# Kernel optimization log

Measured on AMD Instinct MI355X. Metric: run time of the kernel, lower is better.

The kernel has to match this reference:

```python
import jax, jax.numpy as jnp
from jax import lax
import numpy as np

CONF = 0.05   # score threshold
IOU = 0.5     # NMS IoU threshold
IMG = 512.0   # input image size (d0)
PRE_K = 1000  # fixed pre-NMS candidate count (replaces variable-length boolean mask)
MAX_DET = 100 # fixed max detections per image
B, C = 16, 90
CLS_OFF = 4096.0  # batched_nms class offset (> max coordinate)

def _make_anchors():
    # EfficientDet-d0 anchor grid: strides 8..128, anchor_scale=4, 3 scales x 3 ratios
    strides = [8, 16, 32, 64, 128]
    scs = [2.0 ** 0, 2.0 ** (1.0 / 3.0), 2.0 ** (2.0 / 3.0)]
    ratios = [(1.0, 1.0), (1.4, 0.7), (0.7, 1.4)]
    out = []
    for s in strides:
        n = int(512 // s)
        yy, xx = np.meshgrid((np.arange(n) + 0.5) * s, (np.arange(n) + 0.5) * s, indexing='ij')
        cy = yy.reshape(-1); cx = xx.reshape(-1)
        for sc in scs:
            for ry, rx in ratios:
                h = 4.0 * s * sc * ry / 2.0
                w = 4.0 * s * sc * rx / 2.0
                out.append(np.stack([cy - h, cx - w, cy + h, cx + w], -1))  # (y1,x1,y2,x2)
    return jnp.asarray(np.concatenate(out, 0), dtype=jnp.float32)[None]  # [1,49104,4]

def setup_inputs():
    key = jax.random.key(0)
    k1, k2 = jax.random.split(key)
    anchors = _make_anchors()
    A = anchors.shape[1]
    regression = 0.1 * jax.random.normal(k1, (B, A, 4), dtype=jnp.float32)
    classification = jax.random.uniform(k2, (B, A, C), dtype=jnp.float32) ** 8  # sigmoid-like sparse scores
    scales = jnp.ones((B, 2), dtype=jnp.float32)
    pads = jnp.zeros((B, 2), dtype=jnp.float32)
    return {'anchors': anchors, 'regression': regression, 'classification': classification,
            'scales': scales, 'pads': pads}

def _decode(anchors, regression):
    yca = (anchors[..., 0] + anchors[..., 2]) / 2
    xca = (anchors[..., 1] + anchors[..., 3]) / 2
    ha = anchors[..., 2] - anchors[..., 0]
    wa = anchors[..., 3] - anchors[..., 1]
    w = jnp.exp(regression[..., 3]) * wa
    h = jnp.exp(regression[..., 2]) * ha
    yc = regression[..., 0] * ha + yca
    xc = regression[..., 1] * wa + xca
    return jnp.stack([xc - w / 2, yc - h / 2, xc + w / 2, yc + h / 2], axis=2)  # [B,A,4] xyxy

def _iou_mat(b):
    # b: [K,4] xyxy -> [K,K] IoU
    area = jnp.clip(b[:, 2] - b[:, 0], 0) * jnp.clip(b[:, 3] - b[:, 1], 0)
    lt = jnp.maximum(b[:, None, :2], b[None, :, :2])
    rb = jnp.minimum(b[:, None, 2:], b[None, :, 2:])
    wh = jnp.clip(rb - lt, 0)
    inter = wh[..., 0] * wh[..., 1]
    return inter / jnp.maximum(area[:, None] + area[None, :] - inter, 1e-8)

def _nms_keep(boxes, scores):
    # greedy NMS on score-sorted boxes; entries with score<=CONF never kept nor suppress
    K = boxes.shape[0]
    iou = _iou_mat(boxes)
    valid = scores > CONF
    idx = jnp.arange(K)
    def body(i, keep):
        cur = keep[i] & valid[i]
        sup = cur & (iou[i] > IOU) & (idx > i)
        return keep & ~sup
    return lax.fori_loop(0, K, body, valid)

def _per_image(boxes, smax, cls, scale, pad):
    # boxes [A,4], smax [A], cls [A], scale [2] (sy,sx), pad [2] (py,px)
    sc = jnp.where(smax > CONF, smax, -1.0)
    topv, topi = lax.top_k(sc, PRE_K)          # sorted descending
    bk = boxes[topi]                            # [K,4]
    ck = cls[topi]                              # [K]
    boff = bk + (ck.astype(bk.dtype) * CLS_OFF)[:, None]  # class-aware NMS offset
    keep = lax.stop_gradient(_nms_keep(lax.stop_gradient(boff), lax.stop_gradient(topv)))
    sf = jnp.where(keep, topv, -1.0)
    fv, fi = lax.top_k(sf, MAX_DET)
    bf = bk[fi]
    lf = ck[fi]
    valid = fv > CONF
    # undo pad/scale, clip to image (original clips to orig width/height; identity scale/pad here)
    x1 = jnp.clip((bf[:, 0] - pad[1]) / scale[1], 0.0, IMG)
    y1 = jnp.clip((bf[:, 1] - pad[0]) / scale[0], 0.0, IMG)
    x2 = jnp.clip((bf[:, 2] - pad[1]) / scale[1], 0.0, IMG)
    y2 = jnp.clip((bf[:, 3] - pad[0]) / scale[0], 0.0, IMG)
    bfr = jnp.stack([x1, y1, x2, y2], -1)
    bfr = jnp.where(valid[:, None], bfr, 0.0)
    sv = jnp.where(valid, fv, 0.0)
    lfv = jnp.where(valid, lf, -1)
    return bfr, sv, lfv

def reference(anchors, regression, classification, scales, pads):
    boxes = _decode(anchors, regression)            # [B,A,4]
    smax = jnp.max(classification, axis=2)          # [B,A]
    cls = jnp.argmax(classification, axis=2)        # [B,A]
    bf, sv, lf = jax.vmap(_per_image)(boxes, smax, cls, scales, pads)
    out5 = jnp.concatenate([bf, sv[..., None]], axis=-1)  # [B,MAX_DET,5]
    return out5, lf
```

## Files before the change

kernel.cpp:

```cpp
#include <hip/hip_runtime.h>

#define A_N 49104
#define B_N 16
#define C_N 90
#define KP 1024
#define MROWS 1088

__global__ __launch_bounds__(256) void k_score(
    const float* __restrict__ classification,
    float* __restrict__ smax, int* __restrict__ cls) {
  int a = blockIdx.x * 256 + threadIdx.x;
  int b = blockIdx.y;
  if (a >= A_N) return;
  const float2* cp2 = (const float2*)(classification + ((size_t)b * A_N + a) * C_N);
  float m = -1.0f; int am = 0;
#pragma unroll
  for (int k = 0; k < C_N / 2; ++k) {
    float2 v = cp2[k];
    if (v.x > m) { m = v.x; am = 2 * k; }
    if (v.y > m) { m = v.y; am = 2 * k + 1; }
  }
  size_t o = (size_t)b * A_N + a;
  smax[o] = m;
  cls[o] = am;
}

__global__ __launch_bounds__(1024) void k_select(
    const float* __restrict__ smax, const int* __restrict__ cls,
    const float* __restrict__ anchors, const float* __restrict__ regression,
    float* __restrict__ topbox, float* __restrict__ topv, int* __restrict__ topcls,
    unsigned long long* __restrict__ validb) {
  __shared__ unsigned long long cand[2048];
  __shared__ unsigned s_red[16];
  __shared__ unsigned s_tot;
  __shared__ int s_cnt;
  const int tid = threadIdx.x;
  const int b = blockIdx.x;
  const int lane = tid & 63, wv = tid >> 6;
  const float* sm = smax + (size_t)b * A_N;

  unsigned ub[48];
#pragma unroll
  for (int k = 0; k < 48; ++k) {
    int a = tid + k * 1024;
    float s = (a < A_N) ? sm[a] : -1.0f;
    ub[k] = (s > 0.05f) ? __float_as_uint(s) : 0u;
  }

  unsigned lo = __float_as_uint(0.05f) + 1u;
  unsigned hi = __float_as_uint(1.0f) + 1u;
  while (hi - lo > 1u) {
    unsigned mid = lo + ((hi - lo) >> 1);
    int c = 0;
#pragma unroll
    for (int k = 0; k < 48; ++k) c += (ub[k] >= mid) ? 1 : 0;
#pragma unroll
    for (int off = 32; off > 0; off >>= 1) c += __shfl_down(c, off, 64);
    if (lane == 0) s_red[wv] = (unsigned)c;
    __syncthreads();
    if (tid == 0) {
      unsigned tot = 0;
      for (int i = 0; i < 16; ++i) tot += s_red[i];
      s_tot = tot;
    }
    __syncthreads();
    if (s_tot >= 1000u) lo = mid; else hi = mid;
    __syncthreads();
  }
  const unsigned T = lo;

  if (tid == 0) s_cnt = 0;
  __syncthreads();
#pragma unroll
  for (int k = 0; k < 48; ++k) {
    if (ub[k] >= T) {
      int a = tid + k * 1024;
      int p = atomicAdd(&s_cnt, 1);
      if (p < 2048)
        cand[p] = ~(((unsigned long long)ub[k] << 32) |
                    (unsigned long long)(0xFFFFFFFFu - (unsigned)a));
    }
  }
  __syncthreads();
  int cnt = s_cnt; if (cnt > 2048) cnt = 2048;
  for (int i = tid; i < 2048; i += 1024) if (i >= cnt) cand[i] = ~0ULL;
  __syncthreads();

  for (int k = 2; k <= 2048; k <<= 1) {
    for (int j = k >> 1; j > 0; j >>= 1) {
      for (int i = tid; i < 2048; i += 1024) {
        int l = i ^ j;
        if (l > i) {
          unsigned long long vi = cand[i], vl = cand[l];
          if ((vi > vl) == ((i & k) == 0)) { cand[i] = vl; cand[l] = vi; }
        }
      }
      __syncthreads();
    }
  }

  {
    const int t = tid;
    unsigned long long key = ~cand[t];
    unsigned sb = (unsigned)(key >> 32);
    unsigned idxa = 0xFFFFFFFFu - (unsigned)(key & 0xFFFFFFFFull);
    bool v = (t < 1000) && (sb != 0u);
    float b0 = 0.f, b1 = 0.f, b2 = 0.f, b3 = 0.f, sv = -1.0f; int cl = 0;
    if (v) {
      float4 an = ((const float4*)anchors)[idxa];
      float4 rg = ((const float4*)regression)[(size_t)b * A_N + idxa];
      float yca = __fmul_rn(__fadd_rn(an.x, an.z), 0.5f);
      float xca = __fmul_rn(__fadd_rn(an.y, an.w), 0.5f);
      float ha = __fsub_rn(an.z, an.x);
      float wa = __fsub_rn(an.w, an.y);
      float w  = __fmul_rn((float)exp((double)rg.w), wa);
      float h  = __fmul_rn((float)exp((double)rg.z), ha);
      float yc = __fadd_rn(__fmul_rn(rg.x, ha), yca);
      float xc = __fadd_rn(__fmul_rn(rg.y, wa), xca);
      float wh = __fmul_rn(w, 0.5f), hh = __fmul_rn(h, 0.5f);
      b0 = __fsub_rn(xc, wh); b1 = __fsub_rn(yc, hh);
      b2 = __fadd_rn(xc, wh); b3 = __fadd_rn(yc, hh);
      cl = cls[(size_t)b * A_N + idxa];
      sv = __uint_as_float(sb);
    }
    float* tb = topbox + ((size_t)b * KP + t) * 4;
    tb[0] = b0; tb[1] = b1; tb[2] = b2; tb[3] = b3;
    topv[b * KP + t] = sv;
    topcls[b * KP + t] = cl;
  }
  if (tid < 16) {
    unsigned long long vb = 0ULL;
    for (int bit = 0; bit < 64; ++bit) {
      int t = tid * 64 + bit;
      if (t < 1000 && (unsigned)((~cand[t]) >> 32) != 0u) vb |= (1ULL << bit);
    }
    validb[b * 16 + tid] = vb;
  }
}

__global__ __launch_bounds__(256) void k_mask(
    const float* __restrict__ topbox, const int* __restrict__ topcls,
    unsigned long long* __restrict__ mask) {
  __shared__ float sx1[KP], sy1[KP], sx2[KP], sy2[KP], sar[KP];
  const int b = blockIdx.y, rb = blockIdx.x;
  const int tid = threadIdx.x;
  for (int jj = tid; jj < KP; jj += 256) {
    const float* bp = topbox + ((size_t)b * KP + jj) * 4;
    float off = (float)topcls[b * KP + jj] * 4096.0f;
    float x1 = __fadd_rn(bp[0], off), y1 = __fadd_rn(bp[1], off);
    float x2 = __fadd_rn(bp[2], off), y2 = __fadd_rn(bp[3], off);
    sx1[jj] = x1; sy1[jj] = y1; sx2[jj] = x2; sy2[jj] = y2;
    sar[jj] = __fmul_rn(fmaxf(__fsub_rn(x2, x1), 0.0f), fmaxf(__fsub_rn(y2, y1), 0.0f));
  }
  __syncthreads();
  const int wv = tid >> 6, lane = tid & 63;
  for (int task = wv; task < 128; task += 4) {
    const int r = task >> 4, cc = task & 15;
    const int i = rb * 8 + r;
    const int j = cc * 64 + lane;
    float xi1 = sx1[i], yi1 = sy1[i], xi2 = sx2[i], yi2 = sy2[i], ai = sar[i];
    float ltx = fmaxf(xi1, sx1[j]);
    float lty = fmaxf(yi1, sy1[j]);
    float rbx = fminf(xi2, sx2[j]);
    float rby = fminf(yi2, sy2[j]);
    float wx = fmaxf(__fsub_rn(rbx, ltx), 0.0f);
    float wy = fmaxf(__fsub_rn(rby, lty), 0.0f);
    float inter = __fmul_rn(wx, wy);
    float uni = fmaxf(__fsub_rn(__fadd_rn(ai, sar[j]), inter), 1e-8f);
    bool pred = (__fdiv_rn(inter, uni) > 0.5f) && (j > i) && (j < 1000);
    unsigned long long m = __ballot(pred);
    if (lane == 0) mask[((size_t)b * MROWS + i) * 16 + cc] = m;
  }
}

__global__ __launch_bounds__(64) void k_greedy(
    const unsigned long long* __restrict__ mask,
    const float* __restrict__ topv, const float* __restrict__ topbox,
    const int* __restrict__ topcls, const unsigned long long* __restrict__ validb,
    const float* __restrict__ scales, const float* __restrict__ pads,
    float* __restrict__ out) {
  const int b = blockIdx.x;
  const int lane = threadIdx.x;
  const int c = lane & 15, q = lane >> 4;
  const unsigned long long* M = mask + (size_t)b * MROWS * 16;
  unsigned long long remv = ~validb[b * 16 + c];
  unsigned long long ring[16];
#pragma unroll
  for (int t = 0; t < 16; ++t) ring[t] = M[(size_t)(t * 4 + q) * 16 + c];
  __shared__ unsigned long long keepw[16];
  __shared__ int sel[100];
  __shared__ int s_cnt;
#pragma unroll 1
  for (int g = 0; g < 16; ++g) {
#pragma unroll
    for (int t = 0; t < 16; ++t) {
      const int bb = g * 16 + t;
      unsigned long long cur = ring[t];
      ring[t] = M[(size_t)((bb + 16) * 4 + q) * 16 + c];
#pragma unroll
      for (int q2 = 0; q2 < 4; ++q2) {
        const int i = bb * 4 + q2;
        unsigned long long w = __shfl(remv, i >> 6, 64);
        bool kept = ((w >> (i & 63)) & 1ULL) == 0ULL;
        unsigned long long srow = __shfl(cur, q2 * 16 + c, 64);
        if (kept) remv |= srow;
      }
    }
  }
  if (q == 0) keepw[c] = (~remv) & validb[b * 16 + c];
  __syncthreads();
  if (lane == 0) {
    int cnt = 0;
    for (int ci = 0; ci < 16 && cnt < 100; ++ci) {
      unsigned long long w = keepw[ci];
      while (w && cnt < 100) {
        int bit = __builtin_ctzll(w);
        sel[cnt++] = ci * 64 + bit;
        w &= (w - 1ULL);
      }
    }
    s_cnt = cnt;
  }
  __syncthreads();
  const float sy = scales[b * 2 + 0], sxx = scales[b * 2 + 1];
  const float py = pads[b * 2 + 0],  px = pads[b * 2 + 1];
  for (int s = lane; s < 100; s += 64) {
    float o0 = 0, o1 = 0, o2 = 0, o3 = 0, o4 = 0, lf = -1.0f;
    if (s < s_cnt) {
      const int i = sel[s];
      const float* bp = topbox + ((size_t)b * KP + i) * 4;
      o0 = fminf(fmaxf(__fdiv_rn(__fsub_rn(bp[0], px), sxx), 0.0f), 512.0f);
      o1 = fminf(fmaxf(__fdiv_rn(__fsub_rn(bp[1], py), sy ), 0.0f), 512.0f);
      o2 = fminf(fmaxf(__fdiv_rn(__fsub_rn(bp[2], px), sxx), 0.0f), 512.0f);
      o3 = fminf(fmaxf(__fdiv_rn(__fsub_rn(bp[3], py), sy ), 0.0f), 512.0f);
      o4 = topv[b * KP + i];
      lf = (float)topcls[b * KP + i];
    }
    float* op = out + ((size_t)b * 100 + s) * 5;
    op[0] = o0; op[1] = o1; op[2] = o2; op[3] = o3; op[4] = o4;
    out[(size_t)B_N * 500 + b * 100 + s] = lf;
  }
}

extern "C" void kernel_launch(void* const* d_in, const int* in_sizes, int n_in,
                              void* d_out, int out_size, void* d_ws, size_t ws_size,
                              hipStream_t stream) {
  const float* anchors        = (const float*)d_in[0];
  const float* regression     = (const float*)d_in[1];
  const float* classification = (const float*)d_in[2];
  const float* scales         = (const float*)d_in[3];
  const float* pads           = (const float*)d_in[4];
  char* ws = (char*)d_ws;
  float* smax   = (float*)(ws + 0);
  int*   cls    = (int*)  (ws + 3142656);
  float* topbox = (float*)(ws + 6285312);
  float* topv   = (float*)(ws + 6547456);
  int*   topcls = (int*)  (ws + 6612992);
  unsigned long long* validb = (unsigned long long*)(ws + 6678528);
  unsigned long long* mask   = (unsigned long long*)(ws + 6680576);
  float* out = (float*)d_out;

  k_score <<<dim3((A_N + 255) / 256, B_N), 256, 0, stream>>>(classification, smax, cls);
  k_select<<<B_N, 1024, 0, stream>>>(smax, cls, anchors, regression, topbox, topv, topcls, validb);
  k_mask  <<<dim3(125, B_N), 256, 0, stream>>>(topbox, topcls, mask);
  k_greedy<<<B_N, 64, 0, stream>>>(mask, topv, topbox, topcls, validb, scales, pads, out);
}
```

Before: 540.4 us.

## Coalesce score loads via shared tiles and replace threshold bisection with radix histogram

```diff
diff --git a/kernel.cpp b/kernel.cpp
--- a/kernel.cpp
+++ b/kernel.cpp
@@ -5,24 +5,36 @@
 #define C_N 90
 #define KP 1024
 #define MROWS 1088
+#define ANCH 128
 
 __global__ __launch_bounds__(256) void k_score(
     const float* __restrict__ classification,
     float* __restrict__ smax, int* __restrict__ cls) {
-  int a = blockIdx.x * 256 + threadIdx.x;
-  int b = blockIdx.y;
-  if (a >= A_N) return;
-  const float2* cp2 = (const float2*)(classification + ((size_t)b * A_N + a) * C_N);
-  float m = -1.0f; int am = 0;
-#pragma unroll
-  for (int k = 0; k < C_N / 2; ++k) {
-    float2 v = cp2[k];
-    if (v.x > m) { m = v.x; am = 2 * k; }
-    if (v.y > m) { m = v.y; am = 2 * k + 1; }
-  }
-  size_t o = (size_t)b * A_N + a;
-  smax[o] = m;
-  cls[o] = am;
+  __shared__ float sc[ANCH * C_N];
+  const int blk = blockIdx.x, b = blockIdx.y;
+  const int base = blk * ANCH;
+  const int nA = min(ANCH, A_N - base);
+  const int nf4 = (nA * C_N) >> 2;
+  const float4* s4 = (const float4*)(classification + ((size_t)b * A_N + base) * C_N);
+  float4* d4 = (float4*)sc;
+  for (int i = threadIdx.x; i < nf4; i += 256) d4[i] = s4[i];
+  __syncthreads();
+  const int al = threadIdx.x >> 1;
+  const int half = threadIdx.x & 1;
+  if (al < nA) {
+    const float* p = sc + al * C_N + half * 45;
+    float m = -1.0f; int am = 0;
+#pragma unroll
+    for (int k = 0; k < 45; ++k) { float v = p[k]; if (v > m) { m = v; am = k; } }
+    float m2 = __shfl_xor(m, 1, 64);
+    int am2 = __shfl_xor(am, 1, 64);
+    if (half == 0) {
+      float mm = m; int aa = am;
+      if (m2 > mm) { mm = m2; aa = 45 + am2; }
+      size_t o = (size_t)b * A_N + base + al;
+      smax[o] = mm; cls[o] = aa;
+    }
+  }
 }
 
 __global__ __launch_bounds__(1024) void k_select(
@@ -31,8 +43,8 @@
     float* __restrict__ topbox, float* __restrict__ topv, int* __restrict__ topcls,
     unsigned long long* __restrict__ validb) {
   __shared__ unsigned long long cand[2048];
-  __shared__ unsigned s_red[16];
-  __shared__ unsigned s_tot;
+  __shared__ unsigned hist[4096];
+  __shared__ unsigned s_T, s_cntT, s_binCnt, s_done;
   __shared__ int s_cnt;
   const int tid = threadIdx.x;
   const int b = blockIdx.x;
@@ -47,27 +59,59 @@
     ub[k] = (s > 0.05f) ? __float_as_uint(s) : 0u;
   }
 
-  unsigned lo = __float_as_uint(0.05f) + 1u;
-  unsigned hi = __float_as_uint(1.0f) + 1u;
-  while (hi - lo > 1u) {
-    unsigned mid = lo + ((hi - lo) >> 1);
-    int c = 0;
-#pragma unroll
-    for (int k = 0; k < 48; ++k) c += (ub[k] >= mid) ? 1 : 0;
-#pragma unroll
-    for (int off = 32; off > 0; off >>= 1) c += __shfl_down(c, off, 64);
-    if (lane == 0) s_red[wv] = (unsigned)c;
+  unsigned lo = 0x3D4CCCCEu;
+  unsigned width = 0x3F800001u - lo;
+  unsigned baseCnt = 0, T = lo;
+  for (int pass = 0; pass < 4; ++pass) {
+    int sh = 0;
+    while ((((width - 1u) >> sh) + 1u) > 4096u) ++sh;
+    const unsigned nb = ((width - 1u) >> sh) + 1u;
+    for (int i = tid; i < 4096; i += 1024) hist[i] = 0u;
     __syncthreads();
-    if (tid == 0) {
-      unsigned tot = 0;
-      for (int i = 0; i < 16; ++i) tot += s_red[i];
-      s_tot = tot;
+#pragma unroll
+    for (int k = 0; k < 48; ++k) {
+      unsigned u = ub[k];
+      if (u >= lo && (u - lo) < width) atomicAdd(&hist[(u - lo) >> sh], 1u);
     }
     __syncthreads();
-    if (s_tot >= 1000u) lo = mid; else hi = mid;
+    if (wv == 0) {
+      unsigned run = baseCnt; int B = -1; unsigned cnt = 0, binc = 0;
+      for (int start = (int)nb - 64; B < 0; start -= 64) {
+        int idx = start + lane;
+        unsigned v = (idx >= 0 && idx < (int)nb) ? hist[idx] : 0u;
+        unsigned sfx = v;
+        for (int off = 1; off < 64; off <<= 1) {
+          unsigned o = __shfl_down(sfx, off, 64);
+          if (lane + off < 64) sfx += o;
+        }
+        unsigned chunkTot = __shfl(sfx, 0, 64);
+        if (run + chunkTot >= 1000u) {
+          bool cond = (idx >= 0) && (run + sfx >= 1000u);
+          unsigned long long bal = __ballot(cond);
+          int top = 63 - __clzll(bal);
+          B = start + top;
+          cnt = run + __shfl(sfx, top, 64);
+          binc = __shfl(v, top, 64);
+        } else {
+          run += chunkTot;
+        }
+        if (start <= -63 && B < 0) { B = 0; cnt = run; binc = 0; }
+      }
+      if (lane == 0) {
+        s_T = lo + ((unsigned)B << sh);
+        s_cntT = cnt; s_binCnt = binc;
+        s_done = (cnt <= 2048u || sh == 0) ? 1u : 0u;
+      }
+    }
     __syncthreads();
-  }
-  const unsigned T = lo;
+    T = s_T;
+    if (s_done) break;
+    baseCnt = s_cntT - s_binCnt;
+    int sh2 = 0;
+    while ((((width - 1u) >> sh2) + 1u) > 4096u) ++sh2;
+    lo = s_T; width = 1u << sh2;
+    __syncthreads();
+  }
 
   if (tid == 0) s_cnt = 0;
   __syncthreads();
@@ -260,7 +304,7 @@
   unsigned long long* mask   = (unsigned long long*)(ws + 6680576);
   float* out = (float*)d_out;
 
-  k_score <<<dim3((A_N + 255) / 256, B_N), 256, 0, stream>>>(classification, smax, cls);
+  k_score <<<dim3((A_N + ANCH - 1) / ANCH, B_N), 256, 0, stream>>>(classification, smax, cls);
   k_select<<<B_N, 1024, 0, stream>>>(smax, cls, anchors, regression, topbox, topv, topcls, validb);
   k_mask  <<<dim3(125, B_N), 256, 0, stream>>>(topbox, topcls, mask);
   k_greedy<<<B_N, 64, 0, stream>>>(mask, topv, topbox, topcls, validb, scales, pads, out);
```

Measured after the change: 511.1 us. -5.4%, faster.
